# Kernel optimization log

Hardware: AMD Instinct MI355X
Metric: run time of the kernel (lower is better)

## Reference

```python
import jax, jax.numpy as jnp
import numpy as np

N = 20000      # total nodes
E = 320000     # edges (before self loops)
B = 8          # graphs in batch
F_IN = 100
HID = 256
HEADS = 4
DIMS = [(256, 256), (256, 128), (128, 64), (64, 32)]  # (in_dim, out_dim) per level
NEG_SLOPE = 0.2
LN_EPS = 1e-5


def _glorot(k, shape):
    fan = shape[0] + shape[-1]
    return jax.random.normal(k, shape, jnp.float32) * jnp.sqrt(2.0 / fan)


def setup_inputs() -> dict:
    key = jax.random.key(0)
    ks = jax.random.split(key, 32)
    inp = {}
    inp["x"] = jax.random.normal(ks[0], (N, F_IN), jnp.float32)
    inp["edge_index"] = jax.random.randint(ks[1], (2, E), 0, N)
    inp["batch"] = jnp.sort(jax.random.randint(ks[2], (N,), 0, B))
    inp["W_in"] = _glorot(ks[3], (F_IN, HID))
    inp["b_in"] = jnp.zeros((HID,), jnp.float32)
    i = 4
    for l, (di, do) in enumerate(DIMS):
        inp[f"W{l}"] = _glorot(ks[i], (di, HEADS * do)); i += 1
        inp[f"as{l}"] = _glorot(ks[i], (HEADS, do)); i += 1
        inp[f"ad{l}"] = _glorot(ks[i], (HEADS, do)); i += 1
        inp[f"b{l}"] = jnp.zeros((do,), jnp.float32)
        inp[f"g{l}"] = jnp.ones((do,), jnp.float32)
        inp[f"be{l}"] = jnp.zeros((do,), jnp.float32)
    inp["W_out"] = _glorot(ks[i], (DIMS[-1][1], 1))
    inp["b_out"] = jnp.zeros((1,), jnp.float32)
    return inp


def _gat(x, src, dst, W, a_s, a_d, b):
    # PyG GATConv, heads=HEADS, concat=False (head mean), bias after mean
    h = (x @ W).reshape(N, HEADS, -1)              # [N,H,C]
    al_s = (h * a_s).sum(-1)                        # [N,H]
    al_d = (h * a_d).sum(-1)                        # [N,H]
    e = jax.nn.leaky_relu(al_s[src] + al_d[dst], NEG_SLOPE)  # [Etot,H]
    m = jax.ops.segment_max(e, dst, num_segments=N)
    m = jnp.where(jnp.isfinite(m), m, 0.0)
    ex = jnp.exp(e - m[dst])
    den = jax.ops.segment_sum(ex, dst, num_segments=N)
    alpha = ex / (den[dst] + 1e-16)                 # segment softmax over incoming edges
    out = jax.ops.segment_sum(alpha[:, :, None] * h[src], dst, num_segments=N)
    return out.mean(axis=1) + b                     # [N,C]


def _ln(x, g, b):
    mu = x.mean(-1, keepdims=True)
    var = ((x - mu) ** 2).mean(-1, keepdims=True)
    return (x - mu) * jax.lax.rsqrt(var + LN_EPS) * g + b


def _forward(x, edge_index, batch, W_in, b_in, level_params, W_out, b_out):
    loop = jnp.arange(N)
    src = jnp.concatenate([edge_index[0], loop])    # add self loops (GATConv default)
    dst = jnp.concatenate([edge_index[1], loop])
    h = jax.nn.relu(x @ W_in + b_in)
    for (di, do), (W, a_s, a_d, b, g, be) in zip(DIMS, level_params):
        out = _gat(h, src, dst, W, a_s, a_d, b)
        out = jax.nn.relu(out)
        out = _ln(out, g, be)
        # dropout is identity in eval mode
        if di == do:
            out = out + h
        h = out
    cnt = jax.ops.segment_sum(jnp.ones((N,), h.dtype), batch, num_segments=B)
    pooled = jax.ops.segment_sum(h, batch, num_segments=B) / jnp.maximum(cnt, 1.0)[:, None]
    return (pooled @ W_out + b_out)[:, 0]           # [B]


def reference(x, edge_index, batch, W_in, b_in,
              W0, as0, ad0, b0, g0, be0,
              W1, as1, ad1, b1, g1, be1,
              W2, as2, ad2, b2, g2, be2,
              W3, as3, ad3, b3, g3, be3,
              W_out, b_out):
    level_params = [
        (W0, as0, ad0, b0, g0, be0),
        (W1, as1, ad1, b1, g1, be1),
        (W2, as2, ad2, b2, g2, be2),
        (W3, as3, ad3, b3, g3, be3),
    ]
    return _forward(x, edge_index, batch, W_in, b_in, level_params, W_out, b_out)
```

## Files before the change

### kernel.cpp

```cpp
#include <hip/hip_runtime.h>
#include <hip/hip_bf16.h>
#include <cstdint>

constexpr int NN   = 20000;
constexpr int NE   = 320000;
constexpr int ETOT = NE + NN;
constexpr int BG   = 8;
constexpr int FIN  = 100;
constexpr int HID  = 256;
constexpr int H    = 4;
constexpr float SLOPE  = 0.2f;
constexpr float LN_EPS = 1e-5f;

#define DEVFN __device__ __forceinline__

typedef __bf16 bf16x8 __attribute__((ext_vector_type(8)));
typedef float  f32x4  __attribute__((ext_vector_type(4)));
typedef float  f32x2  __attribute__((ext_vector_type(2)));

DEVFN float lrelu(float v) { return v > 0.f ? v : SLOPE * v; }
DEVFN ushort f2bf(float f) {
    unsigned u = __float_as_uint(f);
    return (ushort)((u + 0x7fffu + ((u >> 16) & 1u)) >> 16);
}
DEVFN float bf_lo(unsigned u) { return __uint_as_float(u << 16); }
DEVFN float bf_hi(unsigned u) { return __uint_as_float(u & 0xffff0000u); }
DEVFN float bf2f(unsigned u) { return __uint_as_float(u << 16); }

__global__ void zero_u32(uint32_t* __restrict__ p, int n) {
    int i = blockIdx.x * blockDim.x + threadIdx.x;
    if (i < n) p[i] = 0u;
}

__global__ void count_deg(const int* __restrict__ ei, int* __restrict__ deg) {
    int k = blockIdx.x * blockDim.x + threadIdx.x;
    if (k >= ETOT) return;
    int d = (k < NE) ? ei[NE + k] : (k - NE);
    atomicAdd(&deg[d], 1);
}

__global__ void scan_kernel(const int* __restrict__ deg, int* __restrict__ rowptr) {
    __shared__ int wsum[16];
    __shared__ int woff[16];
    __shared__ int ctot;
    const int lane = threadIdx.x & 63;
    const int wv   = threadIdx.x >> 6;
    int carry = 0;
    for (int base = 0; base < NN; base += 1024) {
        int i = base + threadIdx.x;
        int v = (i < NN) ? deg[i] : 0;
        int s = v;
#pragma unroll
        for (int off = 1; off < 64; off <<= 1) {
            int t = __shfl_up(s, off);
            if (lane >= off) s += t;
        }
        if (lane == 63) wsum[wv] = s;
        __syncthreads();
        if (wv == 0 && lane < 16) {
            int ws = wsum[lane];
            int sc = ws;
#pragma unroll
            for (int off = 1; off < 16; off <<= 1) {
                int t = __shfl_up(sc, off);
                if (lane >= off) sc += t;
            }
            woff[lane] = sc - ws;
            if (lane == 15) ctot = sc;
        }
        __syncthreads();
        if (i < NN) rowptr[i] = carry + woff[wv] + (s - v);
        carry += ctot;
        __syncthreads();
    }
    if (threadIdx.x == 0) rowptr[NN] = carry;
}

__global__ void scatter_edges(const int* __restrict__ ei, const int* __restrict__ rowptr,
                              int* __restrict__ fill, int* __restrict__ esrc) {
    int k = blockIdx.x * blockDim.x + threadIdx.x;
    if (k >= ETOT) return;
    int s, d;
    if (k < NE) { s = ei[k]; d = ei[NE + k]; }
    else        { s = k - NE; d = k - NE; }
    int pos = rowptr[d] + atomicAdd(&fill[d], 1);
    esrc[pos] = s;
}

constexpr int CXN  = NN * 128;
constexpr int CWI  = 256 * 128;
constexpr int CW0  = 1024 * 256;
constexpr int CW1  = 512 * 256;
constexpr int CW2  = 256 * 128;
constexpr int CW3  = 128 * 64;
constexpr int CTOT = CXN + CWI + CW0 + CW1 + CW2 + CW3;

__global__ void conv_all(const float* __restrict__ x, const float* __restrict__ Wi,
                         const float* __restrict__ W0, const float* __restrict__ W1,
                         const float* __restrict__ W2, const float* __restrict__ W3,
                         ushort* __restrict__ xpad, ushort* __restrict__ wti,
                         ushort* __restrict__ wt0, ushort* __restrict__ wt1,
                         ushort* __restrict__ wt2, ushort* __restrict__ wt3) {
    int id = blockIdx.x * blockDim.x + threadIdx.x;
    if (id < CXN) {
        int n = id >> 7, k = id & 127;
        xpad[id] = (k < FIN) ? f2bf(x[(size_t)n * FIN + k]) : (ushort)0;
        return;
    }
    id -= CXN;
    if (id < CWI) { int n = id / 128, k = id - n * 128;
        wti[id] = (k < FIN) ? f2bf(Wi[(size_t)k * 256 + n]) : (ushort)0; return; }
    id -= CWI;
    if (id < CW0) { int n = id / 256, k = id - n * 256;
        wt0[id] = f2bf(W0[(size_t)k * 1024 + n]); return; }
    id -= CW0;
    if (id < CW1) { int n = id / 256, k = id - n * 256;
        wt1[id] = f2bf(W1[(size_t)k * 512 + n]); return; }
    id -= CW1;
    if (id < CW2) { int n = id / 128, k = id - n * 128;
        wt2[id] = f2bf(W2[(size_t)k * 256 + n]); return; }
    id -= CW2;
    if (id < CW3) { int n = id / 64, k = id - n * 64;
        wt3[id] = f2bf(W3[(size_t)k * 128 + n]); return; }
}

template <int K, int NC, int CT, bool BR, bool AL>
__launch_bounds__(256)
__global__ void gemm_mfma(const ushort* __restrict__ A, const ushort* __restrict__ Wt,
                          const float* __restrict__ bias, void* __restrict__ Cout,
                          const float* __restrict__ a_s, const float* __restrict__ a_d,
                          float* __restrict__ al_s, float* __restrict__ al_d, int M) {
    constexpr int LDK = K + 8;
    constexpr int DO_AL = NC / H;
    __shared__ ushort As[64 * LDK];
    __shared__ ushort Bs[64 * LDK];
    const int row0 = blockIdx.x * 64;
    const int colbase = blockIdx.y * (64 * CT);
    const int tid = threadIdx.x;
    constexpr int CH = K / 8;
    for (int c = tid; c < 64 * CH; c += 256) {
        int r = c / CH, cc = c - r * CH;
        int gr = row0 + r;
        uint4 v = make_uint4(0u, 0u, 0u, 0u);
        if (gr < M) v = *(const uint4*)(A + (size_t)gr * K + cc * 8);
        *(uint4*)(&As[r * LDK + cc * 8]) = v;
    }
    const int wave = tid >> 6;
    const int lane = tid & 63;
    const int m = lane & 15;
    const int q = lane >> 4;
    const ushort* ap  = &As[(wave * 16 + m) * LDK + q * 8];
    const ushort* bp0 = &Bs[(0 * 16 + m) * LDK + q * 8];
    const ushort* bp1 = &Bs[(1 * 16 + m) * LDK + q * 8];
    const ushort* bp2 = &Bs[(2 * 16 + m) * LDK + q * 8];
    const ushort* bp3 = &Bs[(3 * 16 + m) * LDK + q * 8];
    const int grow0 = row0 + wave * 16 + q * 4;

    for (int ct = 0; ct < CT; ct++) {
        const int col0 = colbase + ct * 64;
        for (int c = tid; c < 64 * CH; c += 256) {
            int r = c / CH, cc = c - r * CH;
            *(uint4*)(&Bs[r * LDK + cc * 8]) =
                *(const uint4*)(Wt + (size_t)(col0 + r) * K + cc * 8);
        }
        __syncthreads();
        f32x4 acc0 = {0.f, 0.f, 0.f, 0.f}, acc1 = acc0, acc2 = acc0, acc3 = acc0;
#pragma unroll
        for (int kk = 0; kk < K / 32; kk++) {
            bf16x8 a = *(const bf16x8*)(ap + kk * 32);
            acc0 = __builtin_amdgcn_mfma_f32_16x16x32_bf16(a, *(const bf16x8*)(bp0 + kk * 32), acc0, 0, 0, 0);
            acc1 = __builtin_amdgcn_mfma_f32_16x16x32_bf16(a, *(const bf16x8*)(bp1 + kk * 32), acc1, 0, 0, 0);
            acc2 = __builtin_amdgcn_mfma_f32_16x16x32_bf16(a, *(const bf16x8*)(bp2 + kk * 32), acc2, 0, 0, 0);
            acc3 = __builtin_amdgcn_mfma_f32_16x16x32_bf16(a, *(const bf16x8*)(bp3 + kk * 32), acc3, 0, 0, 0);
        }
        if (!AL) {
            ushort* Cb = (ushort*)Cout + (size_t)grow0 * NC + col0 + m;
            float b0 = 0, b1 = 0, b2 = 0, b3 = 0;
            if (BR) {
                b0 = bias[col0 + m];      b1 = bias[col0 + m + 16];
                b2 = bias[col0 + m + 32]; b3 = bias[col0 + m + 48];
            }
#pragma unroll
            for (int r = 0; r < 4; r++) {
                if (grow0 + r < M) {
                    float v0 = acc0[r], v1 = acc1[r], v2 = acc2[r], v3 = acc3[r];
                    if (BR) {
                        v0 = fmaxf(v0 + b0, 0.f); v1 = fmaxf(v1 + b1, 0.f);
                        v2 = fmaxf(v2 + b2, 0.f); v3 = fmaxf(v3 + b3, 0.f);
                    }
                    Cb[(size_t)r * NC + 0]  = f2bf(v0);
                    Cb[(size_t)r * NC + 16] = f2bf(v1);
                    Cb[(size_t)r * NC + 32] = f2bf(v2);
                    Cb[(size_t)r * NC + 48] = f2bf(v3);
                }
            }
        } else {
            uchar* Cb = (uchar*)Cout + (size_t)grow0 * NC + col0 + m;
#pragma unroll
            for (int r = 0; r < 4; r++) {
                if (grow0 + r < M) {
                    int pk01 = __builtin_amdgcn_cvt_pk_fp8_f32(acc0[r], acc1[r], 0, false);
                    int pk23 = __builtin_amdgcn_cvt_pk_fp8_f32(acc2[r], acc3[r], 0, false);
                    Cb[(size_t)r * NC + 0]  = (uchar)(pk01 & 0xff);
                    Cb[(size_t)r * NC + 16] = (uchar)((pk01 >> 8) & 0xff);
                    Cb[(size_t)r * NC + 32] = (uchar)(pk23 & 0xff);
                    Cb[(size_t)r * NC + 48] = (uchar)((pk23 >> 8) & 0xff);
                }
            }
            float asv[4], adv[4];
#pragma unroll
            for (int t = 0; t < 4; t++) {
                int gc = col0 + m + 16 * t;
                asv[t] = a_s[gc];
                adv[t] = a_d[gc];
            }
            const int h_lo = col0 / DO_AL;
            const int h_hi = (col0 + 32) / DO_AL;
#pragma unroll
            for (int r = 0; r < 4; r++) {
                float ps0 = acc0[r] * asv[0] + acc1[r] * asv[1];
                float ps1 = acc2[r] * asv[2] + acc3[r] * asv[3];
                float pd0 = acc0[r] * adv[0] + acc1[r] * adv[1];
                float pd1 = acc2[r] * adv[2] + acc3[r] * adv[3];
#pragma unroll
                for (int off = 1; off < 16; off <<= 1) {
                    ps0 += __shfl_xor(ps0, off);
                    ps1 += __shfl_xor(ps1, off);
                    pd0 += __shfl_xor(pd0, off);
                    pd1 += __shfl_xor(pd1, off);
                }
                if (m == 0 && grow0 + r < M) {
                    if (h_lo == h_hi) {
                        atomicAdd(&al_s[(grow0 + r) * H + h_lo], ps0 + ps1);
                        atomicAdd(&al_d[(grow0 + r) * H + h_lo], pd0 + pd1);
                    } else {
                        atomicAdd(&al_s[(grow0 + r) * H + h_lo], ps0);
                        atomicAdd(&al_s[(grow0 + r) * H + h_hi], ps1);
                        atomicAdd(&al_d[(grow0 + r) * H + h_lo], pd0);
                        atomicAdd(&al_d[(grow0 + r) * H + h_hi], pd1);
                    }
                }
            }
        }
        __syncthreads();
    }
}

__global__ void softmax_csr(const int* __restrict__ rowptr, const int* __restrict__ esrc,
                            const float* __restrict__ al_s, const float* __restrict__ al_d,
                            float4* __restrict__ alpha) {
    int wid = (blockIdx.x * blockDim.x + threadIdx.x) >> 6;
    int lane = threadIdx.x & 63;
    if (wid >= NN) return;
    int p0 = rowptr[wid], p1 = rowptr[wid + 1];
    float4 d4 = ((const float4*)al_d)[wid];
    float m0 = -1e30f, m1 = -1e30f, m2 = -1e30f, m3 = -1e30f;
    for (int p = p0 + lane; p < p1; p += 64) {
        int s = esrc[p];
        float4 s4 = ((const float4*)al_s)[s];
        m0 = fmaxf(m0, lrelu(s4.x + d4.x));
        m1 = fmaxf(m1, lrelu(s4.y + d4.y));
        m2 = fmaxf(m2, lrelu(s4.z + d4.z));
        m3 = fmaxf(m3, lrelu(s4.w + d4.w));
    }
#pragma unroll
    for (int off = 32; off > 0; off >>= 1) {
        m0 = fmaxf(m0, __shfl_xor(m0, off));
        m1 = fmaxf(m1, __shfl_xor(m1, off));
        m2 = fmaxf(m2, __shfl_xor(m2, off));
        m3 = fmaxf(m3, __shfl_xor(m3, off));
    }
    float s0 = 0.f, s1 = 0.f, s2 = 0.f, s3 = 0.f;
    for (int p = p0 + lane; p < p1; p += 64) {
        int s = esrc[p];
        float4 s4 = ((const float4*)al_s)[s];
        s0 += __expf(lrelu(s4.x + d4.x) - m0);
        s1 += __expf(lrelu(s4.y + d4.y) - m1);
        s2 += __expf(lrelu(s4.z + d4.z) - m2);
        s3 += __expf(lrelu(s4.w + d4.w) - m3);
    }
#pragma unroll
    for (int off = 32; off > 0; off >>= 1) {
        s0 += __shfl_xor(s0, off);
        s1 += __shfl_xor(s1, off);
        s2 += __shfl_xor(s2, off);
        s3 += __shfl_xor(s3, off);
    }
    float i0 = 0.25f / (s0 + 1e-16f), i1 = 0.25f / (s1 + 1e-16f);
    float i2 = 0.25f / (s2 + 1e-16f), i3 = 0.25f / (s3 + 1e-16f);
    for (int p = p0 + lane; p < p1; p += 64) {
        int s = esrc[p];
        float4 s4 = ((const float4*)al_s)[s];
        alpha[p] = make_float4(__expf(lrelu(s4.x + d4.x) - m0) * i0,
                               __expf(lrelu(s4.y + d4.y) - m1) * i1,
                               __expf(lrelu(s4.z + d4.z) - m2) * i2,
                               __expf(lrelu(s4.w + d4.w) - m3) * i3);
    }
}

template <int DO, bool RESID>
__launch_bounds__(256)
__global__ void aggregate(const uchar* __restrict__ hproj, const int* __restrict__ rowptr,
                          const int* __restrict__ esrc, const float4* __restrict__ alpha,
                          const float* __restrict__ bias, const float* __restrict__ gamma,
                          const float* __restrict__ beta, const ushort* __restrict__ hprev,
                          ushort* __restrict__ hout) {
    constexpr int HDO = H * DO;
    constexpr int SL  = HDO / 16;
    constexpr int EPI = 64 / SL;
    constexpr int HL  = DO / 16;
    const int wave = threadIdx.x >> 6;
    const int lane = threadIdx.x & 63;
    const int n = blockIdx.x * 4 + wave;
    const int e  = lane / SL;
    const int sl = lane - e * SL;
    const int hsel = sl / HL;
    const int p0 = rowptr[n], p1 = rowptr[n + 1];
    const uint4* hp4 = (const uint4*)hproj;

    f32x2 acc2[8];
#pragma unroll
    for (int j = 0; j < 8; j++) acc2[j] = f32x2{0.f, 0.f};

    auto sel = [&](float4 al) {
        return (hsel == 0) ? al.x : (hsel == 1) ? al.y : (hsel == 2) ? al.z : al.w;
    };
    auto consume = [&](uint4 v, float a) {
        f32x2 ap = {a, a};
        acc2[0] += ap * __builtin_amdgcn_cvt_pk_f32_fp8(v.x, false);
        acc2[1] += ap * __builtin_amdgcn_cvt_pk_f32_fp8(v.x, true);
        acc2[2] += ap * __builtin_amdgcn_cvt_pk_f32_fp8(v.y, false);
        acc2[3] += ap * __builtin_amdgcn_cvt_pk_f32_fp8(v.y, true);
        acc2[4] += ap * __builtin_amdgcn_cvt_pk_f32_fp8(v.z, false);
        acc2[5] += ap * __builtin_amdgcn_cvt_pk_f32_fp8(v.z, true);
        acc2[6] += ap * __builtin_amdgcn_cvt_pk_f32_fp8(v.w, false);
        acc2[7] += ap * __builtin_amdgcn_cvt_pk_f32_fp8(v.w, true);
    };

    int p = p0 + e;
    bool va = p < p1;
    bool vb = (p + EPI) < p1;
    float aa = 0.f, ab = 0.f;
    uint4 ua = make_uint4(0, 0, 0, 0), ub = make_uint4(0, 0, 0, 0);
    if (va) { aa = sel(alpha[p]);       ua = hp4[(size_t)esrc[p] * SL + sl]; }
    if (vb) { ab = sel(alpha[p + EPI]); ub = hp4[(size_t)esrc[p + EPI] * SL + sl]; }

    while (__any(va)) {
        int pa = p + 2 * EPI, pb = p + 3 * EPI;
        bool va2 = pa < p1, vb2 = pb < p1;
        float aa2 = 0.f, ab2 = 0.f;
        uint4 ua2 = make_uint4(0, 0, 0, 0), ub2 = make_uint4(0, 0, 0, 0);
        if (va2) { aa2 = sel(alpha[pa]); ua2 = hp4[(size_t)esrc[pa] * SL + sl]; }
        if (vb2) { ab2 = sel(alpha[pb]); ub2 = hp4[(size_t)esrc[pb] * SL + sl]; }
        if (va) consume(ua, aa);
        if (vb) consume(ub, ab);
        p = pa; va = va2; vb = vb2; aa = aa2; ab = ab2; ua = ua2; ub = ub2;
    }

    float acc[16];
#pragma unroll
    for (int j = 0; j < 8; j++) { acc[2 * j] = acc2[j][0]; acc[2 * j + 1] = acc2[j][1]; }

#pragma unroll
    for (int off = 32; off >= HL; off >>= 1) {
#pragma unroll
        for (int j = 0; j < 16; j++) acc[j] += __shfl_xor(acc[j], off);
    }
    const int c2 = lane & (HL - 1);
    const int cb = c2 * 16;
    float val[16];
    float s = 0.f;
    {
        float4 b0 = *(const float4*)(bias + cb);
        float4 b1 = *(const float4*)(bias + cb + 4);
        float4 b2 = *(const float4*)(bias + cb + 8);
        float4 b3 = *(const float4*)(bias + cb + 12);
        float bb[16] = {b0.x, b0.y, b0.z, b0.w, b1.x, b1.y, b1.z, b1.w,
                        b2.x, b2.y, b2.z, b2.w, b3.x, b3.y, b3.z, b3.w};
#pragma unroll
        for (int j = 0; j < 16; j++) {
            val[j] = fmaxf(acc[j] + bb[j], 0.f);
            s += val[j];
        }
    }
#pragma unroll
    for (int off = 1; off < HL; off <<= 1) s += __shfl_xor(s, off);
    float mu = s / DO;
    float q = 0.f;
#pragma unroll
    for (int j = 0; j < 16; j++) {
        val[j] -= mu;
        q += val[j] * val[j];
    }
#pragma unroll
    for (int off = 1; off < HL; off <<= 1) q += __shfl_xor(q, off);
    float rstd = rsqrtf(q / DO + LN_EPS);

    if (lane < HL) {
        float4 g0 = *(const float4*)(gamma + cb);
        float4 g1 = *(const float4*)(gamma + cb + 4);
        float4 g2 = *(const float4*)(gamma + cb + 8);
        float4 g3 = *(const float4*)(gamma + cb + 12);
        float4 e0 = *(const float4*)(beta + cb);
        float4 e1 = *(const float4*)(beta + cb + 4);
        float4 e2 = *(const float4*)(beta + cb + 8);
        float4 e3 = *(const float4*)(beta + cb + 12);
        float gg[16] = {g0.x, g0.y, g0.z, g0.w, g1.x, g1.y, g1.z, g1.w,
                        g2.x, g2.y, g2.z, g2.w, g3.x, g3.y, g3.z, g3.w};
        float ee[16] = {e0.x, e0.y, e0.z, e0.w, e1.x, e1.y, e1.z, e1.w,
                        e2.x, e2.y, e2.z, e2.w, e3.x, e3.y, e3.z, e3.w};
        float o[16];
#pragma unroll
        for (int j = 0; j < 16; j++) o[j] = val[j] * rstd * gg[j] + ee[j];
        if (RESID) {
            const uint4* pv = (const uint4*)(hprev + (size_t)n * DO + cb);
            uint4 r0 = pv[0], r1 = pv[1];
            unsigned rr[8] = {r0.x, r0.y, r0.z, r0.w, r1.x, r1.y, r1.z, r1.w};
#pragma unroll
            for (int j = 0; j < 8; j++) {
                o[2 * j]     += bf_lo(rr[j]);
                o[2 * j + 1] += bf_hi(rr[j]);
            }
        }
        unsigned w[8];
#pragma unroll
        for (int j = 0; j < 8; j++)
            w[j] = (unsigned)f2bf(o[2 * j]) | ((unsigned)f2bf(o[2 * j + 1]) << 16);
        uint4* op = (uint4*)(hout + (size_t)n * DO + cb);
        op[0] = make_uint4(w[0], w[1], w[2], w[3]);
        op[1] = make_uint4(w[4], w[5], w[6], w[7]);
    }
}

__global__ void pool_accum2(const ushort* __restrict__ h, const int* __restrict__ batch,
                            float* __restrict__ pooled, float* __restrict__ cnt) {
    __shared__ float lp[BG * 32];
    __shared__ float lc[BG];
    for (int i = threadIdx.x; i < BG * 32; i += blockDim.x) lp[i] = 0.f;
    if (threadIdx.x < BG) lc[threadIdx.x] = 0.f;
    __syncthreads();
    int c = threadIdx.x & 31;
    int rb = threadIdx.x >> 5;
    for (int n = blockIdx.x * 8 + rb; n < NN; n += gridDim.x * 8) {
        int b = batch[n];
        atomicAdd(&lp[b * 32 + c], bf2f((unsigned)h[(size_t)n * 32 + c]));
        if (c == 0) atomicAdd(&lc[b], 1.f);
    }
    __syncthreads();
    for (int i = threadIdx.x; i < BG * 32; i += blockDim.x) atomicAdd(&pooled[i], lp[i]);
    if (threadIdx.x < BG) atomicAdd(&cnt[threadIdx.x], lc[threadIdx.x]);
}

__global__ void final_out(const float* __restrict__ pooled, const float* __restrict__ cnt,
                          const float* __restrict__ Wo, const float* __restrict__ bo,
                          float* __restrict__ out) {
    int b = threadIdx.x;
    if (b < BG) {
        float inv = 1.f / fmaxf(cnt[b], 1.f);
        float acc = 0.f;
        for (int c = 0; c < 32; c++) acc += pooled[b * 32 + c] * inv * Wo[c];
        out[b] = acc + bo[0];
    }
}

extern "C" void kernel_launch(void* const* d_in, const int* in_sizes, int n_in,
                              void* d_out, int out_size, void* d_ws, size_t ws_size,
                              hipStream_t stream) {
    const float* x     = (const float*)d_in[0];
    const int*   ei    = (const int*)d_in[1];
    const int*   batch = (const int*)d_in[2];
    const float* Wi    = (const float*)d_in[3];
    const float* bi    = (const float*)d_in[4];
    const float* Wl[4]  = {(const float*)d_in[5],  (const float*)d_in[11], (const float*)d_in[17], (const float*)d_in[23]};
    const float* Asl[4] = {(const float*)d_in[6],  (const float*)d_in[12], (const float*)d_in[18], (const float*)d_in[24]};
    const float* Adl[4] = {(const float*)d_in[7],  (const float*)d_in[13], (const float*)d_in[19], (const float*)d_in[25]};
    const float* Bl[4]  = {(const float*)d_in[8],  (const float*)d_in[14], (const float*)d_in[20], (const float*)d_in[26]};
    const float* Gl[4]  = {(const float*)d_in[9],  (const float*)d_in[15], (const float*)d_in[21], (const float*)d_in[27]};
    const float* Bel[4] = {(const float*)d_in[10], (const float*)d_in[16], (const float*)d_in[22], (const float*)d_in[28]};
    const float* Wo = (const float*)d_in[29];
    const float* bo = (const float*)d_in[30];

    char* p = (char*)d_ws;
    auto take = [&](size_t bytes) -> void* {
        void* r = (void*)p;
        p += (bytes + 255) & ~(size_t)255;
        return r;
    };
    ushort*   hAbf   = (ushort*)take((size_t)NN * HID * 2);
    ushort*   hBbf   = (ushort*)take((size_t)NN * HID * 2);
    uchar*    hproj  = (uchar*)take((size_t)NN * H * HID);
    ushort*   xpad   = (ushort*)take((size_t)NN * 128 * 2);
    int*      rowptr = (int*)take((size_t)(NN + 1) * 4);
    int*      esrc   = (int*)take((size_t)ETOT * 4);
    float4*   alpha  = (float4*)take((size_t)ETOT * 16);
    ushort*   wti    = (ushort*)take((size_t)CWI * 2);
    ushort*   wt0    = (ushort*)take((size_t)CW0 * 2);
    ushort*   wt1    = (ushort*)take((size_t)CW1 * 2);
    ushort*   wt2    = (ushort*)take((size_t)CW2 * 2);
    ushort*   wt3    = (ushort*)take((size_t)CW3 * 2);
    char*     zbase  = p;
    int*      deg    = (int*)take((size_t)NN * 4);
    int*      fill   = (int*)take((size_t)NN * 4);
    float*    pooled = (float*)take((size_t)BG * 32 * 4);
    float*    cnt    = (float*)take((size_t)BG * 4);
    float*    als[4], *ald[4];
    for (int l = 0; l < 4; l++) {
        als[l] = (float*)take((size_t)NN * H * 4);
        ald[l] = (float*)take((size_t)NN * H * 4);
    }
    const int zcount = (int)((p - zbase) / 4);
    (void)ws_size; (void)n_in; (void)in_sizes; (void)out_size;

    const int ZB = 256;
    const int egrid = (ETOT + ZB - 1) / ZB;
    const int mtiles = (NN + 63) / 64;
    const int sgrid = (NN * 64 + 255) / 256;
    const int agrid = NN / 4;

    zero_u32<<<(zcount + ZB - 1) / ZB, ZB, 0, stream>>>((uint32_t*)zbase, zcount);
    conv_all<<<(CTOT + ZB - 1) / ZB, ZB, 0, stream>>>(x, Wi, Wl[0], Wl[1], Wl[2], Wl[3],
                                                      xpad, wti, wt0, wt1, wt2, wt3);
    count_deg<<<egrid, ZB, 0, stream>>>(ei, deg);
    scan_kernel<<<1, 1024, 0, stream>>>(deg, rowptr);
    scatter_edges<<<egrid, ZB, 0, stream>>>(ei, rowptr, fill, esrc);

    gemm_mfma<128, 256, 2, true, false><<<dim3(mtiles, 2), 256, 0, stream>>>(
        xpad, wti, bi, hAbf, nullptr, nullptr, nullptr, nullptr, NN);

    gemm_mfma<256, 1024, 4, false, true><<<dim3(mtiles, 4), 256, 0, stream>>>(
        hAbf, wt0, nullptr, hproj, Asl[0], Adl[0], als[0], ald[0], NN);
    softmax_csr<<<sgrid, 256, 0, stream>>>(rowptr, esrc, als[0], ald[0], alpha);
    aggregate<256, true><<<agrid, 256, 0, stream>>>(hproj, rowptr, esrc, alpha,
                                                    Bl[0], Gl[0], Bel[0], hAbf, hBbf);
    gemm_mfma<256, 512, 4, false, true><<<dim3(mtiles, 2), 256, 0, stream>>>(
        hBbf, wt1, nullptr, hproj, Asl[1], Adl[1], als[1], ald[1], NN);
    softmax_csr<<<sgrid, 256, 0, stream>>>(rowptr, esrc, als[1], ald[1], alpha);
    aggregate<128, false><<<agrid, 256, 0, stream>>>(hproj, rowptr, esrc, alpha,
                                                     Bl[1], Gl[1], Bel[1], nullptr, hAbf);
    gemm_mfma<128, 256, 4, false, true><<<dim3(mtiles, 1), 256, 0, stream>>>(
        hAbf, wt2, nullptr, hproj, Asl[2], Adl[2], als[2], ald[2], NN);
    softmax_csr<<<sgrid, 256, 0, stream>>>(rowptr, esrc, als[2], ald[2], alpha);
    aggregate<64, false><<<agrid, 256, 0, stream>>>(hproj, rowptr, esrc, alpha,
                                                    Bl[2], Gl[2], Bel[2], nullptr, hBbf);
    gemm_mfma<64, 128, 2, false, true><<<dim3(mtiles, 1), 256, 0, stream>>>(
        hBbf, wt3, nullptr, hproj, Asl[3], Adl[3], als[3], ald[3], NN);
    softmax_csr<<<sgrid, 256, 0, stream>>>(rowptr, esrc, als[3], ald[3], alpha);
    aggregate<32, false><<<agrid, 256, 0, stream>>>(hproj, rowptr, esrc, alpha,
                                                    Bl[3], Gl[3], Bel[3], nullptr, hAbf);

    pool_accum2<<<80, 256, 0, stream>>>(hAbf, batch, pooled, cnt);
    final_out<<<1, 64, 0, stream>>>(pooled, cnt, Wo, bo, (float*)d_out);
}
```

Before: 574.5 us.

## Fuse edge softmax into aggregation kernel and fold degree count into conversion

The separate per-level softmax_csr kernel is removed. Each aggregation wave now computes the per-destination max and denominator over incoming edges itself, then recomputes each edge's alpha on the fly from the source and destination attention scores. This drops the write and reread of a float4 alpha per edge per level and four kernel launches. In exchange each aggregate wave runs two extra reduction passes over its edges and does a gather plus an exp per edge for every slice. The degree-counting kernel is also merged into the conversion kernel to save one launch.

```diff
diff --git a/kernel.cpp b/kernel.cpp
--- a/kernel.cpp
+++ b/kernel.cpp
@@ -30,13 +30,6 @@
 __global__ void zero_u32(uint32_t* __restrict__ p, int n) {
     int i = blockIdx.x * blockDim.x + threadIdx.x;
     if (i < n) p[i] = 0u;
-}
-
-__global__ void count_deg(const int* __restrict__ ei, int* __restrict__ deg) {
-    int k = blockIdx.x * blockDim.x + threadIdx.x;
-    if (k >= ETOT) return;
-    int d = (k < NE) ? ei[NE + k] : (k - NE);
-    atomicAdd(&deg[d], 1);
 }
 
 __global__ void scan_kernel(const int* __restrict__ deg, int* __restrict__ rowptr) {
@@ -94,10 +87,12 @@
 constexpr int CW2  = 256 * 128;
 constexpr int CW3  = 128 * 64;
 constexpr int CTOT = CXN + CWI + CW0 + CW1 + CW2 + CW3;
+constexpr int CALL = CTOT + ETOT;
 
 __global__ void conv_all(const float* __restrict__ x, const float* __restrict__ Wi,
                          const float* __restrict__ W0, const float* __restrict__ W1,
                          const float* __restrict__ W2, const float* __restrict__ W3,
+                         const int* __restrict__ ei, int* __restrict__ deg,
                          ushort* __restrict__ xpad, ushort* __restrict__ wti,
                          ushort* __restrict__ wt0, ushort* __restrict__ wt1,
                          ushort* __restrict__ wt2, ushort* __restrict__ wt3) {
@@ -122,6 +117,11 @@
     id -= CW2;
     if (id < CW3) { int n = id / 64, k = id - n * 64;
         wt3[id] = f2bf(W3[(size_t)k * 128 + n]); return; }
+    id -= CW3;
+    if (id < ETOT) {
+        int d = (id < NE) ? ei[NE + id] : (id - NE);
+        atomicAdd(&deg[d], 1);
+    }
 }
 
 template <int K, int NC, int CT, bool BR, bool AL>
@@ -246,62 +246,11 @@
     }
 }
 
-__global__ void softmax_csr(const int* __restrict__ rowptr, const int* __restrict__ esrc,
-                            const float* __restrict__ al_s, const float* __restrict__ al_d,
-                            float4* __restrict__ alpha) {
-    int wid = (blockIdx.x * blockDim.x + threadIdx.x) >> 6;
-    int lane = threadIdx.x & 63;
-    if (wid >= NN) return;
-    int p0 = rowptr[wid], p1 = rowptr[wid + 1];
-    float4 d4 = ((const float4*)al_d)[wid];
-    float m0 = -1e30f, m1 = -1e30f, m2 = -1e30f, m3 = -1e30f;
-    for (int p = p0 + lane; p < p1; p += 64) {
-        int s = esrc[p];
-        float4 s4 = ((const float4*)al_s)[s];
-        m0 = fmaxf(m0, lrelu(s4.x + d4.x));
-        m1 = fmaxf(m1, lrelu(s4.y + d4.y));
-        m2 = fmaxf(m2, lrelu(s4.z + d4.z));
-        m3 = fmaxf(m3, lrelu(s4.w + d4.w));
-    }
-#pragma unroll
-    for (int off = 32; off > 0; off >>= 1) {
-        m0 = fmaxf(m0, __shfl_xor(m0, off));
-        m1 = fmaxf(m1, __shfl_xor(m1, off));
-        m2 = fmaxf(m2, __shfl_xor(m2, off));
-        m3 = fmaxf(m3, __shfl_xor(m3, off));
-    }
-    float s0 = 0.f, s1 = 0.f, s2 = 0.f, s3 = 0.f;
-    for (int p = p0 + lane; p < p1; p += 64) {
-        int s = esrc[p];
-        float4 s4 = ((const float4*)al_s)[s];
-        s0 += __expf(lrelu(s4.x + d4.x) - m0);
-        s1 += __expf(lrelu(s4.y + d4.y) - m1);
-        s2 += __expf(lrelu(s4.z + d4.z) - m2);
-        s3 += __expf(lrelu(s4.w + d4.w) - m3);
-    }
-#pragma unroll
-    for (int off = 32; off > 0; off >>= 1) {
-        s0 += __shfl_xor(s0, off);
-        s1 += __shfl_xor(s1, off);
-        s2 += __shfl_xor(s2, off);
-        s3 += __shfl_xor(s3, off);
-    }
-    float i0 = 0.25f / (s0 + 1e-16f), i1 = 0.25f / (s1 + 1e-16f);
-    float i2 = 0.25f / (s2 + 1e-16f), i3 = 0.25f / (s3 + 1e-16f);
-    for (int p = p0 + lane; p < p1; p += 64) {
-        int s = esrc[p];
-        float4 s4 = ((const float4*)al_s)[s];
-        alpha[p] = make_float4(__expf(lrelu(s4.x + d4.x) - m0) * i0,
-                               __expf(lrelu(s4.y + d4.y) - m1) * i1,
-                               __expf(lrelu(s4.z + d4.z) - m2) * i2,
-                               __expf(lrelu(s4.w + d4.w) - m3) * i3);
-    }
-}
-
 template <int DO, bool RESID>
 __launch_bounds__(256)
 __global__ void aggregate(const uchar* __restrict__ hproj, const int* __restrict__ rowptr,
-                          const int* __restrict__ esrc, const float4* __restrict__ alpha,
+                          const int* __restrict__ esrc,
+                          const float* __restrict__ al_s, const float* __restrict__ al_d,
                           const float* __restrict__ bias, const float* __restrict__ gamma,
                           const float* __restrict__ beta, const ushort* __restrict__ hprev,
                           ushort* __restrict__ hout) {
@@ -317,13 +266,53 @@
     const int hsel = sl / HL;
     const int p0 = rowptr[n], p1 = rowptr[n + 1];
     const uint4* hp4 = (const uint4*)hproj;
+    const float4 d4 = ((const float4*)al_d)[n];
+
+    float m0 = -1e30f, m1 = -1e30f, m2 = -1e30f, m3 = -1e30f;
+    for (int p = p0 + lane; p < p1; p += 64) {
+        int s = esrc[p];
+        float4 s4 = ((const float4*)al_s)[s];
+        m0 = fmaxf(m0, lrelu(s4.x + d4.x));
+        m1 = fmaxf(m1, lrelu(s4.y + d4.y));
+        m2 = fmaxf(m2, lrelu(s4.z + d4.z));
+        m3 = fmaxf(m3, lrelu(s4.w + d4.w));
+    }
+#pragma unroll
+    for (int off = 32; off > 0; off >>= 1) {
+        m0 = fmaxf(m0, __shfl_xor(m0, off));
+        m1 = fmaxf(m1, __shfl_xor(m1, off));
+        m2 = fmaxf(m2, __shfl_xor(m2, off));
+        m3 = fmaxf(m3, __shfl_xor(m3, off));
+    }
+    float dn0 = 0.f, dn1 = 0.f, dn2 = 0.f, dn3 = 0.f;
+    for (int p = p0 + lane; p < p1; p += 64) {
+        int s = esrc[p];
+        float4 s4 = ((const float4*)al_s)[s];
+        dn0 += __expf(lrelu(s4.x + d4.x) - m0);
+        dn1 += __expf(lrelu(s4.y + d4.y) - m1);
+        dn2 += __expf(lrelu(s4.z + d4.z) - m2);
+        dn3 += __expf(lrelu(s4.w + d4.w) - m3);
+    }
+#pragma unroll
+    for (int off = 32; off > 0; off >>= 1) {
+        dn0 += __shfl_xor(dn0, off);
+        dn1 += __shfl_xor(dn1, off);
+        dn2 += __shfl_xor(dn2, off);
+        dn3 += __shfl_xor(dn3, off);
+    }
+    const float dh = (hsel == 0) ? d4.x : (hsel == 1) ? d4.y : (hsel == 2) ? d4.z : d4.w;
+    const float mh = (hsel == 0) ? m0 : (hsel == 1) ? m1 : (hsel == 2) ? m2 : m3;
+    const float ih = 0.25f / (((hsel == 0) ? dn0 : (hsel == 1) ? dn1 : (hsel == 2) ? dn2 : dn3) + 1e-16f);
 
     f32x2 acc2[8];
 #pragma unroll
     for (int j = 0; j < 8; j++) acc2[j] = f32x2{0.f, 0.f};
 
-    auto sel = [&](float4 al) {
-        return (hsel == 0) ? al.x : (hsel == 1) ? al.y : (hsel == 2) ? al.z : al.w;
+    auto mkalpha = [&](int p) {
+        int s = esrc[p];
+        float4 s4 = ((const float4*)al_s)[s];
+        float sh = (hsel == 0) ? s4.x : (hsel == 1) ? s4.y : (hsel == 2) ? s4.z : s4.w;
+        return __expf(lrelu(sh + dh) - mh) * ih;
     };
     auto consume = [&](uint4 v, float a) {
         f32x2 ap = {a, a};
@@ -342,16 +331,16 @@
     bool vb = (p + EPI) < p1;
     float aa = 0.f, ab = 0.f;
     uint4 ua = make_uint4(0, 0, 0, 0), ub = make_uint4(0, 0, 0, 0);
-    if (va) { aa = sel(alpha[p]);       ua = hp4[(size_t)esrc[p] * SL + sl]; }
-    if (vb) { ab = sel(alpha[p + EPI]); ub = hp4[(size_t)esrc[p + EPI] * SL + sl]; }
+    if (va) { aa = mkalpha(p);       ua = hp4[(size_t)esrc[p] * SL + sl]; }
+    if (vb) { ab = mkalpha(p + EPI); ub = hp4[(size_t)esrc[p + EPI] * SL + sl]; }
 
     while (__any(va)) {
         int pa = p + 2 * EPI, pb = p + 3 * EPI;
         bool va2 = pa < p1, vb2 = pb < p1;
         float aa2 = 0.f, ab2 = 0.f;
         uint4 ua2 = make_uint4(0, 0, 0, 0), ub2 = make_uint4(0, 0, 0, 0);
-        if (va2) { aa2 = sel(alpha[pa]); ua2 = hp4[(size_t)esrc[pa] * SL + sl]; }
-        if (vb2) { ab2 = sel(alpha[pb]); ub2 = hp4[(size_t)esrc[pb] * SL + sl]; }
+        if (va2) { aa2 = mkalpha(pa); ua2 = hp4[(size_t)esrc[pa] * SL + sl]; }
+        if (vb2) { ab2 = mkalpha(pb); ub2 = hp4[(size_t)esrc[pb] * SL + sl]; }
         if (va) consume(ua, aa);
         if (vb) consume(ub, ab);
         p = pa; va = va2; vb = vb2; aa = aa2; ab = ab2; ua = ua2; ub = ub2;
@@ -492,7 +481,6 @@
     ushort*   xpad   = (ushort*)take((size_t)NN * 128 * 2);
     int*      rowptr = (int*)take((size_t)(NN + 1) * 4);
     int*      esrc   = (int*)take((size_t)ETOT * 4);
-    float4*   alpha  = (float4*)take((size_t)ETOT * 16);
     ushort*   wti    = (ushort*)take((size_t)CWI * 2);
     ushort*   wt0    = (ushort*)take((size_t)CW0 * 2);
     ushort*   wt1    = (ushort*)take((size_t)CW1 * 2);
@@ -514,13 +502,12 @@
     const int ZB = 256;
     const int egrid = (ETOT + ZB - 1) / ZB;
     const int mtiles = (NN + 63) / 64;
-    const int sgrid = (NN * 64 + 255) / 256;
     const int agrid = NN / 4;
 
     zero_u32<<<(zcount + ZB - 1) / ZB, ZB, 0, stream>>>((uint32_t*)zbase, zcount);
-    conv_all<<<(CTOT + ZB - 1) / ZB, ZB, 0, stream>>>(x, Wi, Wl[0], Wl[1], Wl[2], Wl[3],
+    conv_all<<<(CALL + ZB - 1) / ZB, ZB, 0, stream>>>(x, Wi, Wl[0], Wl[1], Wl[2], Wl[3],
+                                                      ei, deg,
                                                       xpad, wti, wt0, wt1, wt2, wt3);
-    count_deg<<<egrid, ZB, 0, stream>>>(ei, deg);
     scan_kernel<<<1, 1024, 0, stream>>>(deg, rowptr);
     scatter_edges<<<egrid, ZB, 0, stream>>>(ei, rowptr, fill, esrc);
 
@@ -529,23 +516,19 @@
 
     gemm_mfma<256, 1024, 4, false, true><<<dim3(mtiles, 4), 256, 0, stream>>>(
         hAbf, wt0, nullptr, hproj, Asl[0], Adl[0], als[0], ald[0], NN);
-    softmax_csr<<<sgrid, 256, 0, stream>>>(rowptr, esrc, als[0], ald[0], alpha);
-    aggregate<256, true><<<agrid, 256, 0, stream>>>(hproj, rowptr, esrc, alpha,
+    aggregate<256, true><<<agrid, 256, 0, stream>>>(hproj, rowptr, esrc, als[0], ald[0],
                                                     Bl[0], Gl[0], Bel[0], hAbf, hBbf);
     gemm_mfma<256, 512, 4, false, true><<<dim3(mtiles, 2), 256, 0, stream>>>(
         hBbf, wt1, nullptr, hproj, Asl[1], Adl[1], als[1], ald[1], NN);
-    softmax_csr<<<sgrid, 256, 0, stream>>>(rowptr, esrc, als[1], ald[1], alpha);
-    aggregate<128, false><<<agrid, 256, 0, stream>>>(hproj, rowptr, esrc, alpha,
+    aggregate<128, false><<<agrid, 256, 0, stream>>>(hproj, rowptr, esrc, als[1], ald[1],
                                                      Bl[1], Gl[1], Bel[1], nullptr, hAbf);
     gemm_mfma<128, 256, 4, false, true><<<dim3(mtiles, 1), 256, 0, stream>>>(
         hAbf, wt2, nullptr, hproj, Asl[2], Adl[2], als[2], ald[2], NN);
-    softmax_csr<<<sgrid, 256, 0, stream>>>(rowptr, esrc, als[2], ald[2], alpha);
-    aggregate<64, false><<<agrid, 256, 0, stream>>>(hproj, rowptr, esrc, alpha,
+    aggregate<64, false><<<agrid, 256, 0, stream>>>(hproj, rowptr, esrc, als[2], ald[2],
                                                     Bl[2], Gl[2], Bel[2], nullptr, hBbf);
     gemm_mfma<64, 128, 2, false, true><<<dim3(mtiles, 1), 256, 0, stream>>>(
         hBbf, wt3, nullptr, hproj, Asl[3], Adl[3], als[3], ald[3], NN);
-    softmax_csr<<<sgrid, 256, 0, stream>>>(rowptr, esrc, als[3], ald[3], alpha);
-    aggregate<32, false><<<agrid, 256, 0, stream>>>(hproj, rowptr, esrc, alpha,
+    aggregate<32, false><<<agrid, 256, 0, stream>>>(hproj, rowptr, esrc, als[3], ald[3],
                                                     Bl[3], Gl[3], Bel[3], nullptr, hAbf);
 
     pool_accum2<<<80, 256, 0, stream>>>(hAbf, batch, pooled, cnt);
```

Result: no change. 578.2 us (+0.6%).
